# Kernel optimization log

Measured on AMD Instinct MI355X. Metric: run time of the kernel, lower is better.

Reference implementation:

```python
import math
import jax, jax.numpy as jnp
import numpy as np

B, L, H = 8, 2048, 256


def setup_inputs() -> dict:
    key = jax.random.key(0)
    k1, k2, k3, k4, k5 = jax.random.split(key, 5)
    inputs = jax.random.normal(k1, (B, L, H), dtype=jnp.float32)
    scale = 1.0 / math.sqrt(H)
    Wq = jax.random.normal(k2, (H, H), dtype=jnp.float32) * scale
    Wk = jax.random.normal(k3, (H, H), dtype=jnp.float32) * scale
    Wv = jax.random.normal(k4, (H, H), dtype=jnp.float32) * scale
    lens = jax.random.randint(k5, (B,), L // 2, L + 1)
    lens = lens.at[0].set(L)  # original assumes max(lens) == L
    return {"inputs": inputs, "Wq": Wq, "Wk": Wk, "Wv": Wv, "lens": lens}


def reference(inputs, Wq, Wk, Wv, lens):
    # nn.Linear(bias=False): y = x @ W.T
    Q = jnp.einsum('blh,oh->blo', inputs, Wq)
    K = jnp.einsum('blh,oh->blo', inputs, Wk)
    V = jnp.einsum('blh,oh->blo', inputs, Wv)
    d = Q.shape[-1]
    alpha = jnp.einsum('bqd,bkd->bqk', Q, K) / math.sqrt(d)  # [B, L, L]
    # key-padding mask: [B, 1, L] broadcast over query dim (matches expand)
    mask = (jnp.arange(L)[None, :] < lens[:, None])[:, None, :]
    NEG = jnp.float32(-2.0 ** 31)
    alpha = jnp.where(mask, alpha, NEG)
    alpha = jax.nn.softmax(alpha, axis=2)
    out = jnp.einsum('bqk,bkd->bqd', alpha, V)
    return out
```

## Files before the change

### kernel.cpp

```cpp
#include <hip/hip_runtime.h>

#define BB 8
#define LL 2048
#define DD 256

typedef _Float16 half8 __attribute__((ext_vector_type(8)));
typedef float floatx4 __attribute__((ext_vector_type(4)));
typedef unsigned short ushort8 __attribute__((ext_vector_type(8)));

__device__ inline unsigned short f2h(float f) {
  _Float16 h = (_Float16)f;
  return __builtin_bit_cast(unsigned short, h);
}

__global__ __launch_bounds__(512) void proj(
    const float* __restrict__ x, const float* __restrict__ Wq,
    const float* __restrict__ Wk, const float* __restrict__ Wv,
    unsigned short* __restrict__ Qb, unsigned short* __restrict__ Kb,
    unsigned short* __restrict__ VT) {
  __shared__ __attribute__((aligned(16))) unsigned char smem[69632];
  unsigned short* Ws = (unsigned short*)smem;
  unsigned short* tile = (unsigned short*)(smem + 32768);
  const int t = threadIdx.x;
  const int wave = t >> 6, lane = t & 63, quad = lane >> 4, m16 = lane & 15;
  const int ot = wave >> 1, p = wave & 1;
  const int l0g = blockIdx.x * 64;
  const int b = l0g >> 11, lb = l0g & 2047;

  half8 xf[2][8];
#pragma unroll
  for (int j = 0; j < 2; ++j) {
    const float* xp =
        x + (size_t)(l0g + (p * 2 + j) * 16 + m16) * DD + quad * 8;
#pragma unroll
    for (int kb = 0; kb < 8; ++kb) {
      float4 a = *(const float4*)(xp + kb * 32);
      float4 c = *(const float4*)(xp + kb * 32 + 4);
      ushort8 u = {f2h(a.x), f2h(a.y), f2h(a.z), f2h(a.w),
                   f2h(c.x), f2h(c.y), f2h(c.z), f2h(c.w)};
      xf[j][kb] = __builtin_bit_cast(half8, u);
    }
  }

  float4 wA[4], wB[4];
#define LOADW(G)                                                              \
  {                                                                           \
    const int mat_ = (G) >> 2, og_ = (G)&3;                                   \
    const float* Wm = (mat_ == 0) ? Wq : (mat_ == 1) ? Wk : Wv;               \
    _Pragma("unroll") for (int c = 0; c < 4; ++c) {                           \
      int ch = c * 512 + t, row = ch >> 5, cc = ch & 31;                      \
      const float* s = Wm + (size_t)(og_ * 64 + row) * DD + cc * 8;           \
      wA[c] = *(const float4*)s;                                              \
      wB[c] = *(const float4*)(s + 4);                                        \
    }                                                                         \
  }

  LOADW(0);
  asm volatile("" ::: "memory");

  for (int g = 0; g < 12; ++g) {
    const int mat = g >> 2, og = g & 3;
    __syncthreads();
#pragma unroll
    for (int c = 0; c < 4; ++c) {
      int ch = c * 512 + t, row = ch >> 5, cc = ch & 31;
      ushort8 u = {f2h(wA[c].x), f2h(wA[c].y), f2h(wA[c].z), f2h(wA[c].w),
                   f2h(wB[c].x), f2h(wB[c].y), f2h(wB[c].z), f2h(wB[c].w)};
      *(ushort8*)&Ws[row * 256 + ((cc ^ (row & 7)) << 3)] = u;
    }
    __syncthreads();
    if (g < 11) {
      LOADW(g + 1);
      asm volatile("" ::: "memory");
    }

    floatx4 acc[2] = {{0, 0, 0, 0}, {0, 0, 0, 0}};
    if (mat < 2) {
#pragma unroll
      for (int kb = 0; kb < 8; ++kb) {
        half8 wf = __builtin_bit_cast(
            half8, *(const ushort8*)&Ws[(ot * 16 + m16) * 256 +
                                        (((kb * 4 + quad) ^ (m16 & 7)) << 3)]);
        acc[0] = __builtin_amdgcn_mfma_f32_16x16x32_f16(xf[0][kb], wf,
                                                        acc[0], 0, 0, 0);
        acc[1] = __builtin_amdgcn_mfma_f32_16x16x32_f16(xf[1][kb], wf,
                                                        acc[1], 0, 0, 0);
      }
#pragma unroll
      for (int j = 0; j < 2; ++j)
#pragma unroll
        for (int r = 0; r < 4; ++r)
          tile[((p * 2 + j) * 16 + quad * 4 + r) * 264 + og * 64 + ot * 16 +
               m16] = f2h(acc[j][r]);
    } else {
#pragma unroll
      for (int kb = 0; kb < 8; ++kb) {
        half8 wf = __builtin_bit_cast(
            half8, *(const ushort8*)&Ws[(ot * 16 + m16) * 256 +
                                        (((kb * 4 + quad) ^ (m16 & 7)) << 3)]);
        acc[0] = __builtin_amdgcn_mfma_f32_16x16x32_f16(wf, xf[0][kb],
                                                        acc[0], 0, 0, 0);
        acc[1] = __builtin_amdgcn_mfma_f32_16x16x32_f16(wf, xf[1][kb],
                                                        acc[1], 0, 0, 0);
      }
#pragma unroll
      for (int j = 0; j < 2; ++j)
#pragma unroll
        for (int r = 0; r < 4; ++r)
          tile[(og * 64 + ot * 16 + quad * 4 + r) * 72 + (p * 2 + j) * 16 +
               m16] = f2h(acc[j][r]);
    }

    if (og == 3) {
      __syncthreads();
      if (mat < 2) {
        unsigned short* Out = mat ? Kb : Qb;
        const int row = t >> 3, c0 = (t & 7) * 8;
#pragma unroll
        for (int i = 0; i < 4; ++i) {
          ushort8 v = *(const ushort8*)&tile[row * 264 + c0 + i * 64];
          *(ushort8*)(Out + (size_t)(l0g + row) * DD + c0 + i * 64) = v;
        }
      } else {
#pragma unroll
        for (int c = 0; c < 4; ++c) {
          int ch = c * 512 + t, d = ch >> 3, lc = (ch & 7) * 8;
          ushort8 v = *(const ushort8*)&tile[d * 72 + lc];
          *(ushort8*)(VT + ((size_t)(b * DD + d)) * LL + lb + lc) = v;
        }
      }
    }
  }
#undef LOADW
}

__global__ __launch_bounds__(512, 1) void attn(
    const unsigned short* __restrict__ Qb, const unsigned short* __restrict__ Kb,
    const unsigned short* __restrict__ VT, const int* __restrict__ lens,
    float* __restrict__ out) {
  __shared__ __attribute__((aligned(16))) unsigned char smem[149504];
  const int t = threadIdx.x;
  const int wave = t >> 6, lane = t & 63, quad = lane >> 4, m16 = lane & 15;
  const int grp = wave >> 2, qw = wave & 3, tgl = t & 255;
  unsigned short* Ks = (unsigned short*)(smem + grp * 32768);
  unsigned short* Vs = (unsigned short*)(smem + 65536 + grp * 32768);
  unsigned short* Pw = (unsigned short*)(smem + 131072 + wave * 2304);

  const int b = blockIdx.x;
  const int q0 = blockIdx.y * 64;
  const int len = lens[b];
  const size_t baseQK = (size_t)b * LL * DD;
  const size_t baseVT = (size_t)b * DD * LL;

  half8 qf[8];
  {
    const unsigned short* qrow =
        Qb + baseQK + (size_t)(q0 + qw * 16 + m16) * DD + quad * 8;
    for (int kb = 0; kb < 8; ++kb)
      qf[kb] = __builtin_bit_cast(half8, *(const ushort8*)(qrow + kb * 32));
  }

  floatx4 O[16];
  for (int i = 0; i < 16; ++i) O[i] = (floatx4){0, 0, 0, 0};
  float mrow[4] = {-1e30f, -1e30f, -1e30f, -1e30f};
  float lrow[4] = {0.f, 0.f, 0.f, 0.f};

  ushort8 kreg[8], vreg[8];
  const unsigned short* kbase = Kb + baseQK;
  const unsigned short* vbase = VT + baseVT;

#define LOAD_TILES(KV0)                                                      \
  {                                                                          \
    const unsigned short* kp = kbase + (size_t)(KV0)*DD;                     \
    for (int c = 0; c < 8; ++c)                                              \
      kreg[c] = *(const ushort8*)(kp + (tgl + c * 256) * 8);                 \
    for (int c = 0; c < 8; ++c) {                                            \
      int ch = tgl + c * 256;                                                \
      vreg[c] = *(const ushort8*)(vbase + (size_t)(ch >> 3) * LL + (KV0) +   \
                                  (ch & 7) * 8);                             \
    }                                                                        \
  }

  const int T = (len + 127) >> 7;
  LOAD_TILES(grp * 64);
  asm volatile("" ::: "memory");

  for (int it = 0; it < T; ++it) {
    const int kv0 = it * 128 + grp * 64;
    __syncthreads();
    for (int c = 0; c < 8; ++c) {
      int ch = tgl + c * 256, row = ch >> 5, cc = ch & 31;
      *(ushort8*)&Ks[row * 256 + (cc ^ (row & 7)) * 8] = kreg[c];
    }
    for (int c = 0; c < 8; ++c) {
      int ch = tgl + c * 256, d = ch >> 3, cc = ch & 7;
      *(ushort8*)&Vs[d * 64 + (cc ^ (d & 7)) * 8] = vreg[c];
    }
    __syncthreads();
    if (it + 1 < T) {
      LOAD_TILES(kv0 + 128);
      asm volatile("" ::: "memory");
    }

    if (kv0 < len) {
      floatx4 s[4];
      for (int n = 0; n < 4; ++n) s[n] = (floatx4){0, 0, 0, 0};
      __builtin_amdgcn_s_setprio(1);
      for (int kb = 0; kb < 8; ++kb)
        for (int n = 0; n < 4; ++n) {
          half8 kf = __builtin_bit_cast(
              half8, *(const ushort8*)&Ks[(n * 16 + m16) * 256 +
                                          (((kb * 4 + quad) ^ (m16 & 7)) * 8)]);
          s[n] = __builtin_amdgcn_mfma_f32_16x16x32_f16(qf[kb], kf, s[n], 0, 0, 0);
        }
      __builtin_amdgcn_s_setprio(0);
      float sv[4][4];
      for (int n = 0; n < 4; ++n) {
        bool valid = (kv0 + n * 16 + m16) < len;
        for (int r = 0; r < 4; ++r)
          sv[n][r] = valid ? s[n][r] * 0.0625f : -1e30f;
      }
      float al[4];
      for (int r = 0; r < 4; ++r) {
        float v = fmaxf(fmaxf(sv[0][r], sv[1][r]), fmaxf(sv[2][r], sv[3][r]));
        v = fmaxf(v, __shfl_xor(v, 1));
        v = fmaxf(v, __shfl_xor(v, 2));
        v = fmaxf(v, __shfl_xor(v, 4));
        v = fmaxf(v, __shfl_xor(v, 8));
        float mn = fmaxf(mrow[r], v);
        al[r] = __expf(mrow[r] - mn);
        mrow[r] = mn;
        float sum = 0.f;
        for (int n = 0; n < 4; ++n) {
          float p = __expf(sv[n][r] - mn);
          Pw[(quad * 4 + r) * 72 + n * 16 + m16] = f2h(p);
          sum += p;
        }
        sum += __shfl_xor(sum, 1);
        sum += __shfl_xor(sum, 2);
        sum += __shfl_xor(sum, 4);
        sum += __shfl_xor(sum, 8);
        lrow[r] = lrow[r] * al[r] + sum;
      }
      for (int i = 0; i < 16; ++i)
        for (int r = 0; r < 4; ++r) O[i][r] *= al[r];
      half8 pf0 = __builtin_bit_cast(half8,
                                     *(const ushort8*)&Pw[m16 * 72 + quad * 8]);
      half8 pf1 = __builtin_bit_cast(
          half8, *(const ushort8*)&Pw[m16 * 72 + 32 + quad * 8]);
      __builtin_amdgcn_s_setprio(1);
      for (int nb = 0; nb < 16; ++nb) {
        half8 vf0 = __builtin_bit_cast(
            half8, *(const ushort8*)&Vs[(nb * 16 + m16) * 64 +
                                        ((quad ^ (m16 & 7)) * 8)]);
        O[nb] = __builtin_amdgcn_mfma_f32_16x16x32_f16(pf0, vf0, O[nb], 0, 0, 0);
        half8 vf1 = __builtin_bit_cast(
            half8, *(const ushort8*)&Vs[(nb * 16 + m16) * 64 +
                                        (((4 + quad) ^ (m16 & 7)) * 8)]);
        O[nb] = __builtin_amdgcn_mfma_f32_16x16x32_f16(pf1, vf1, O[nb], 0, 0, 0);
      }
      __builtin_amdgcn_s_setprio(0);
    }
  }
#undef LOAD_TILES

  __syncthreads();
  float* Om = (float*)(smem) + qw * 4112;
  float* ml = (float*)(smem + 65792) + qw * 32;
  if (grp == 1) {
    for (int nb = 0; nb < 16; ++nb)
      for (int r = 0; r < 4; ++r)
        Om[(quad * 4 + r) * 257 + nb * 16 + m16] = O[nb][r];
    if (m16 == 0)
      for (int r = 0; r < 4; ++r) {
        ml[(quad * 4 + r) * 2] = mrow[r];
        ml[(quad * 4 + r) * 2 + 1] = lrow[r];
      }
  }
  __syncthreads();
  if (grp == 0) {
    float a[4], bf[4], inv[4];
    for (int r = 0; r < 4; ++r) {
      float mB = ml[(quad * 4 + r) * 2];
      float lB = ml[(quad * 4 + r) * 2 + 1];
      float m = fmaxf(mrow[r], mB);
      a[r] = __expf(mrow[r] - m);
      bf[r] = __expf(mB - m);
      inv[r] = 1.f / (lrow[r] * a[r] + lB * bf[r]);
    }
    for (int nb = 0; nb < 16; ++nb)
      for (int r = 0; r < 4; ++r) {
        float ob = Om[(quad * 4 + r) * 257 + nb * 16 + m16];
        out[baseQK + (size_t)(q0 + qw * 16 + quad * 4 + r) * DD + nb * 16 +
            m16] = (O[nb][r] * a[r] + ob * bf[r]) * inv[r];
      }
  }
}

extern "C" void kernel_launch(void* const* d_in, const int* in_sizes, int n_in,
                              void* d_out, int out_size, void* d_ws, size_t ws_size,
                              hipStream_t stream) {
  const float* x = (const float*)d_in[0];
  const float* Wq = (const float*)d_in[1];
  const float* Wk = (const float*)d_in[2];
  const float* Wv = (const float*)d_in[3];
  const int* lens = (const int*)d_in[4];
  unsigned short* Qb = (unsigned short*)d_ws;
  unsigned short* Kb = Qb + (size_t)BB * LL * DD;
  unsigned short* VT = Kb + (size_t)BB * LL * DD;
  float* out = (float*)d_out;

  proj<<<256, 512, 0, stream>>>(x, Wq, Wk, Wv, Qb, Kb, VT);
  attn<<<dim3(8, 32), 512, 0, stream>>>(Qb, Kb, VT, lens, out);
}
```

Measured before the change: 168.9 us.

## Stage K/V tiles via direct global-to-LDS loads with double buffering

Replaces the register-staged K/V loads and LDS stores with global_load_lds direct copies into a double-buffered LDS ring. Each wave group now handles 32 keys per iteration instead of 64, with matching swizzles for the K and V layouts. Rescaling of O is skipped when no row max grew anywhere in the wave. The aim is to cut VGPR pressure and the LDS store instructions and to overlap the next tile's fetch with compute. In exchange, each MFMA step processes smaller tiles and there are twice as many iterations and barriers.

```diff
diff --git a/kernel.cpp b/kernel.cpp
--- a/kernel.cpp
+++ b/kernel.cpp
@@ -12,6 +12,11 @@
   _Float16 h = (_Float16)f;
   return __builtin_bit_cast(unsigned short, h);
 }
+
+#define GLD16(src, ldsbase)                                                    \
+  __builtin_amdgcn_global_load_lds(                                           \
+      (const __attribute__((address_space(1))) unsigned int*)(src),           \
+      (__attribute__((address_space(3))) unsigned int*)(ldsbase), 16, 0, 0)
 
 __global__ __launch_bounds__(512) void proj(
     const float* __restrict__ x, const float* __restrict__ Wq,
@@ -138,102 +143,115 @@
     const unsigned short* __restrict__ Qb, const unsigned short* __restrict__ Kb,
     const unsigned short* __restrict__ VT, const int* __restrict__ lens,
     float* __restrict__ out) {
-  __shared__ __attribute__((aligned(16))) unsigned char smem[149504];
+  __shared__ __attribute__((aligned(16))) unsigned char smem[141312];
   const int t = threadIdx.x;
   const int wave = t >> 6, lane = t & 63, quad = lane >> 4, m16 = lane & 15;
-  const int grp = wave >> 2, qw = wave & 3, tgl = t & 255;
-  unsigned short* Ks = (unsigned short*)(smem + grp * 32768);
-  unsigned short* Vs = (unsigned short*)(smem + 65536 + grp * 32768);
-  unsigned short* Pw = (unsigned short*)(smem + 131072 + wave * 2304);
+  const int grp = wave >> 2, qw = wave & 3;
+  unsigned short* Pw = (unsigned short*)(smem + 131072 + wave * 1280);
 
   const int b = blockIdx.x;
   const int q0 = blockIdx.y * 64;
   const int len = lens[b];
   const size_t baseQK = (size_t)b * LL * DD;
   const size_t baseVT = (size_t)b * DD * LL;
+  const unsigned short* kbase = Kb + baseQK;
+  const unsigned short* vbase = VT + baseVT;
 
   half8 qf[8];
   {
     const unsigned short* qrow =
         Qb + baseQK + (size_t)(q0 + qw * 16 + m16) * DD + quad * 8;
+#pragma unroll
     for (int kb = 0; kb < 8; ++kb)
       qf[kb] = __builtin_bit_cast(half8, *(const ushort8*)(qrow + kb * 32));
   }
 
   floatx4 O[16];
+#pragma unroll
   for (int i = 0; i < 16; ++i) O[i] = (floatx4){0, 0, 0, 0};
   float mrow[4] = {-1e30f, -1e30f, -1e30f, -1e30f};
   float lrow[4] = {0.f, 0.f, 0.f, 0.f};
 
-  ushort8 kreg[8], vreg[8];
-  const unsigned short* kbase = Kb + baseQK;
-  const unsigned short* vbase = VT + baseVT;
-
-#define LOAD_TILES(KV0)                                                      \
-  {                                                                          \
-    const unsigned short* kp = kbase + (size_t)(KV0)*DD;                     \
-    for (int c = 0; c < 8; ++c)                                              \
-      kreg[c] = *(const ushort8*)(kp + (tgl + c * 256) * 8);                 \
-    for (int c = 0; c < 8; ++c) {                                            \
-      int ch = tgl + c * 256;                                                \
-      vreg[c] = *(const ushort8*)(vbase + (size_t)(ch >> 3) * LL + (KV0) +   \
-                                  (ch & 7) * 8);                             \
-    }                                                                        \
-  }
-
-  const int T = (len + 127) >> 7;
-  LOAD_TILES(grp * 64);
-  asm volatile("" ::: "memory");
+#define VSWZ(d) (((d) ^ ((d) >> 2)) & 3)
+#define STAGE(BUF, KV0)                                                       \
+  {                                                                           \
+    _Pragma("unroll") for (int c = 0; c < 4; ++c) {                           \
+      int i = c * 512 + t;                                                    \
+      int g = i >> 10, ci = i & 1023, row = ci >> 5, pp = ci & 31;            \
+      const unsigned short* src = kbase +                                     \
+          (size_t)((KV0) + g * 32 + row) * DD + ((pp ^ (row & 7)) << 3);      \
+      GLD16(src, smem + (BUF)*32768 + i * 16);                                \
+    }                                                                         \
+    _Pragma("unroll") for (int c = 0; c < 4; ++c) {                           \
+      int i = c * 512 + t;                                                    \
+      int g = i >> 10, ci = i & 1023, d = ci >> 2, pp = ci & 3;               \
+      const unsigned short* src = vbase + (size_t)d * LL + (KV0) + g * 32 +   \
+                                  ((pp ^ VSWZ(d)) << 3);                      \
+      GLD16(src, smem + 65536 + (BUF)*32768 + i * 16);                        \
+    }                                                                         \
+  }
+
+  const int T = (len + 63) >> 6;
+  STAGE(0, 0);
+  __syncthreads();
 
   for (int it = 0; it < T; ++it) {
-    const int kv0 = it * 128 + grp * 64;
-    __syncthreads();
-    for (int c = 0; c < 8; ++c) {
-      int ch = tgl + c * 256, row = ch >> 5, cc = ch & 31;
-      *(ushort8*)&Ks[row * 256 + (cc ^ (row & 7)) * 8] = kreg[c];
-    }
-    for (int c = 0; c < 8; ++c) {
-      int ch = tgl + c * 256, d = ch >> 3, cc = ch & 7;
-      *(ushort8*)&Vs[d * 64 + (cc ^ (d & 7)) * 8] = vreg[c];
-    }
-    __syncthreads();
+    const int cur = it & 1;
     if (it + 1 < T) {
-      LOAD_TILES(kv0 + 128);
+      STAGE(cur ^ 1, (it + 1) * 64);
       asm volatile("" ::: "memory");
     }
-
-    if (kv0 < len) {
-      floatx4 s[4];
-      for (int n = 0; n < 4; ++n) s[n] = (floatx4){0, 0, 0, 0};
+    const int kvg = it * 64 + grp * 32;
+
+    if (kvg < len) {
+      const unsigned short* Kg =
+          (const unsigned short*)(smem + cur * 32768 + grp * 16384);
+      const unsigned short* Vg =
+          (const unsigned short*)(smem + 65536 + cur * 32768 + grp * 16384);
+
+      floatx4 s[2] = {{0, 0, 0, 0}, {0, 0, 0, 0}};
       __builtin_amdgcn_s_setprio(1);
-      for (int kb = 0; kb < 8; ++kb)
-        for (int n = 0; n < 4; ++n) {
+#pragma unroll
+      for (int kb = 0; kb < 8; ++kb) {
+#pragma unroll
+        for (int n = 0; n < 2; ++n) {
           half8 kf = __builtin_bit_cast(
-              half8, *(const ushort8*)&Ks[(n * 16 + m16) * 256 +
-                                          (((kb * 4 + quad) ^ (m16 & 7)) * 8)]);
+              half8, *(const ushort8*)&Kg[(n * 16 + m16) * 256 +
+                                          (((kb * 4 + quad) ^ (m16 & 7)) << 3)]);
           s[n] = __builtin_amdgcn_mfma_f32_16x16x32_f16(qf[kb], kf, s[n], 0, 0, 0);
         }
+      }
       __builtin_amdgcn_s_setprio(0);
-      float sv[4][4];
-      for (int n = 0; n < 4; ++n) {
-        bool valid = (kv0 + n * 16 + m16) < len;
+
+      float sv[2][4];
+      bool vld[2];
+#pragma unroll
+      for (int n = 0; n < 2; ++n) vld[n] = (kvg + n * 16 + m16) < len;
+#pragma unroll
+      for (int n = 0; n < 2; ++n)
+#pragma unroll
         for (int r = 0; r < 4; ++r)
-          sv[n][r] = valid ? s[n][r] * 0.0625f : -1e30f;
-      }
+          sv[n][r] = vld[n] ? s[n][r] * 0.0625f : -1e30f;
+
       float al[4];
+      bool grew = false;
+#pragma unroll
       for (int r = 0; r < 4; ++r) {
-        float v = fmaxf(fmaxf(sv[0][r], sv[1][r]), fmaxf(sv[2][r], sv[3][r]));
+        float v = fmaxf(sv[0][r], sv[1][r]);
         v = fmaxf(v, __shfl_xor(v, 1));
         v = fmaxf(v, __shfl_xor(v, 2));
         v = fmaxf(v, __shfl_xor(v, 4));
         v = fmaxf(v, __shfl_xor(v, 8));
-        float mn = fmaxf(mrow[r], v);
-        al[r] = __expf(mrow[r] - mn);
+        float mo = mrow[r];
+        float mn = fmaxf(mo, v);
+        grew |= (mn > mo);
+        al[r] = __expf(mo - mn);
         mrow[r] = mn;
         float sum = 0.f;
-        for (int n = 0; n < 4; ++n) {
+#pragma unroll
+        for (int n = 0; n < 2; ++n) {
           float p = __expf(sv[n][r] - mn);
-          Pw[(quad * 4 + r) * 72 + n * 16 + m16] = f2h(p);
+          Pw[(quad * 4 + r) * 40 + n * 16 + m16] = f2h(p);
           sum += p;
         }
         sum += __shfl_xor(sum, 1);
@@ -242,36 +260,41 @@
         sum += __shfl_xor(sum, 8);
         lrow[r] = lrow[r] * al[r] + sum;
       }
-      for (int i = 0; i < 16; ++i)
-        for (int r = 0; r < 4; ++r) O[i][r] *= al[r];
-      half8 pf0 = __builtin_bit_cast(half8,
-                                     *(const ushort8*)&Pw[m16 * 72 + quad * 8]);
-      half8 pf1 = __builtin_bit_cast(
-          half8, *(const ushort8*)&Pw[m16 * 72 + 32 + quad * 8]);
+      if (__any(grew)) {
+#pragma unroll
+        for (int i = 0; i < 16; ++i)
+#pragma unroll
+          for (int r = 0; r < 4; ++r) O[i][r] *= al[r];
+      }
+
+      half8 pf = __builtin_bit_cast(half8,
+                                    *(const ushort8*)&Pw[m16 * 40 + quad * 8]);
       __builtin_amdgcn_s_setprio(1);
+#pragma unroll
       for (int nb = 0; nb < 16; ++nb) {
-        half8 vf0 = __builtin_bit_cast(
-            half8, *(const ushort8*)&Vs[(nb * 16 + m16) * 64 +
-                                        ((quad ^ (m16 & 7)) * 8)]);
-        O[nb] = __builtin_amdgcn_mfma_f32_16x16x32_f16(pf0, vf0, O[nb], 0, 0, 0);
-        half8 vf1 = __builtin_bit_cast(
-            half8, *(const ushort8*)&Vs[(nb * 16 + m16) * 64 +
-                                        (((4 + quad) ^ (m16 & 7)) * 8)]);
-        O[nb] = __builtin_amdgcn_mfma_f32_16x16x32_f16(pf1, vf1, O[nb], 0, 0, 0);
+        const int d = nb * 16 + m16;
+        half8 vf = __builtin_bit_cast(
+            half8, *(const ushort8*)&Vg[d * 32 + ((quad ^ VSWZ(d)) << 3)]);
+        O[nb] = __builtin_amdgcn_mfma_f32_16x16x32_f16(pf, vf, O[nb], 0, 0, 0);
       }
       __builtin_amdgcn_s_setprio(0);
     }
-  }
-#undef LOAD_TILES
+    __syncthreads();
+  }
+#undef STAGE
+#undef VSWZ
 
   __syncthreads();
   float* Om = (float*)(smem) + qw * 4112;
   float* ml = (float*)(smem + 65792) + qw * 32;
   if (grp == 1) {
+#pragma unroll
     for (int nb = 0; nb < 16; ++nb)
+#pragma unroll
       for (int r = 0; r < 4; ++r)
         Om[(quad * 4 + r) * 257 + nb * 16 + m16] = O[nb][r];
     if (m16 == 0)
+#pragma unroll
       for (int r = 0; r < 4; ++r) {
         ml[(quad * 4 + r) * 2] = mrow[r];
         ml[(quad * 4 + r) * 2 + 1] = lrow[r];
@@ -280,6 +303,7 @@
   __syncthreads();
   if (grp == 0) {
     float a[4], bf[4], inv[4];
+#pragma unroll
     for (int r = 0; r < 4; ++r) {
       float mB = ml[(quad * 4 + r) * 2];
       float lB = ml[(quad * 4 + r) * 2 + 1];
@@ -288,7 +312,9 @@
       bf[r] = __expf(mB - m);
       inv[r] = 1.f / (lrow[r] * a[r] + lB * bf[r]);
     }
+#pragma unroll
     for (int nb = 0; nb < 16; ++nb)
+#pragma unroll
       for (int r = 0; r < 4; ++r) {
         float ob = Om[(quad * 4 + r) * 257 + nb * 16 + m16];
         out[baseQK + (size_t)(q0 + qw * 16 + quad * 4 + r) * DD + nb * 16 +
```

New measurement: 182.7 us. 1.08x slower.
